# Kernel tuning notes

Hardware: AMD Instinct MI355X
Metric: run time of the kernel (lower is better)

Reference implementation:

```python
import jax, jax.numpy as jnp
import numpy as np

B, D, E, K = 8192, 1024, 8, 5  # batch, in_dim, num_size_classes, num_depth_classes
H = max(64, D)                 # hidden = max(64, in_dim)
EPS = 1e-8


def ordinal_logits_to_probs(logits, num_classes):
    # logits: [B, K-1] cumulative ordinal logits -> [B, K] class probs
    q = jax.nn.sigmoid(logits)
    probs = jnp.concatenate(
        [1.0 - q[:, :1], q[:, :-1] - q[:, 1:], q[:, -1:]], axis=1
    )  # [B, K]
    probs = jnp.clip(probs, EPS)
    return probs / jnp.clip(probs.sum(axis=1, keepdims=True), EPS)


def setup_inputs() -> dict:
    key = jax.random.key(0)
    kx, ks, k1, k2 = jax.random.split(key, 4)
    x = jax.random.normal(kx, (B, D), dtype=jnp.float32)
    size_idx = jax.random.randint(ks, (B,), 0, E, dtype=jnp.int64)
    # per-expert 2-layer MLP params: Linear(D,H) -> ReLU -> Linear(H,K-1)
    W1 = jax.random.normal(k1, (E, D, H), dtype=jnp.float32) / np.sqrt(D)
    b1 = jnp.zeros((E, H), dtype=jnp.float32)
    W2 = jax.random.normal(k2, (E, H, K - 1), dtype=jnp.float32) / np.sqrt(H)
    b2 = jnp.zeros((E, K - 1), dtype=jnp.float32)
    return {"x": x, "size_idx": size_idx, "W1": W1, "b1": b1, "W2": W2, "b2": b2}


def reference(x, size_idx, W1, b1, W2, b2):
    # Hard routing: each token gets the output of expert size_idx[b].
    # Dense all-expert compute + per-token select (same math as mask/gather/scatter,
    # dropout is inference-mode identity).
    h = jax.nn.relu(jnp.einsum('bd,edh->beh', x, W1) + b1)      # [B, E, H]
    all_logits = jnp.einsum('beh,ehk->bek', h, W2) + b2          # [B, E, K-1]
    idx = size_idx.astype(jnp.int32)[:, None, None]              # [B, 1, 1]
    logits = jnp.take_along_axis(all_logits, idx, axis=1)[:, 0]  # [B, K-1]
    probs = ordinal_logits_to_probs(logits, K)                   # [B, K]
    return logits, probs
```

## Files before the change

kernel.cpp:

```cpp
#include <hip/hip_runtime.h>
#include <cstdint>
#include <cstddef>

#define Bn 8192
#define Dn 1024
#define Hn 1024
#define En 8
#define MT 128
#define MTILES (PERM_N / MT)
#define PERM_N (Bn + En * MT)
#define NB 16

#define NXB 4096
#define NWB 2048
#define XB0 1
#define WB0 (XB0 + NXB)
#define TOTB (WB0 + NWB)

typedef unsigned short u16;
typedef __bf16 bf16x8 __attribute__((ext_vector_type(8)));
typedef float f32x4 __attribute__((ext_vector_type(4)));
typedef unsigned short ushort8 __attribute__((ext_vector_type(8)));

__device__ __forceinline__ u16 f2bf(float f) {
  unsigned int u = __float_as_uint(f);
  unsigned int r = u + 0x7fffu + ((u >> 16) & 1u);
  return (u16)(r >> 16);
}

__device__ __forceinline__ void gld16(const void* g, void* l) {
  __builtin_amdgcn_global_load_lds(
      (const __attribute__((address_space(1))) void*)g,
      (__attribute__((address_space(3))) void*)l, 16, 0, 0);
}

#define PIPE_BARRIER_VM4() do {                    \
    asm volatile("" ::: "memory");                 \
    __builtin_amdgcn_s_waitcnt(0x0F74);            \
    __builtin_amdgcn_s_barrier();                  \
    asm volatile("" ::: "memory");                 \
  } while (0)
#define PIPE_BARRIER_VM0() do {                    \
    asm volatile("" ::: "memory");                 \
    __builtin_amdgcn_s_waitcnt(0x0F70);            \
    __builtin_amdgcn_s_barrier();                  \
    asm volatile("" ::: "memory");                 \
  } while (0)

__global__ __launch_bounds__(256) void prep_k(
    const float* __restrict__ x, const int* __restrict__ sidx,
    const float* __restrict__ W1,
    u16* __restrict__ xb, u16* __restrict__ w1t,
    int* __restrict__ off, int* __restrict__ perm) {
  int bid = blockIdx.x;
  int t = threadIdx.x;

  if (bid == 0) {
    __shared__ int hist[4][En];
    __shared__ int base[4][En];
    __shared__ int eoff[En + 1];
    int wv = t >> 6;
    if (t < 4 * En) ((int*)hist)[t] = 0;
#pragma unroll
    for (int i = 0; i < PERM_N / 256; i++) perm[t + i * 256] = -1;
    __syncthreads();
    int e32[32], r32[32];
#pragma unroll
    for (int i = 0; i < 32; i++) {
      int e = sidx[t + i * 256];
      e32[i] = e;
      r32[i] = atomicAdd(&hist[wv][e], 1);
    }
    __syncthreads();
    if (t < En) {
      int s = 0;
      for (int w = 0; w < 4; w++) { base[w][t] = s; s += hist[w][t]; }
      hist[0][t] = s;
    }
    __syncthreads();
    if (t == 0) {
      int o = 0;
      for (int e = 0; e < En; e++) {
        eoff[e] = o; off[e] = o;
        o += (hist[0][e] + MT - 1) & ~(MT - 1);
      }
      eoff[En] = o; off[En] = o;
    }
    __syncthreads();
#pragma unroll
    for (int i = 0; i < 32; i++) {
      int e = e32[i];
      perm[eoff[e] + base[wv][e] + r32[i]] = t + i * 256;
    }
  } else if (bid < WB0) {
    size_t idx = ((size_t)(bid - XB0) * 256 + t) * 8;
    const float* src = x + idx;
    float4 a = *(const float4*)src;
    float4 b = *(const float4*)(src + 4);
    ushort8 o;
    o[0] = f2bf(a.x); o[1] = f2bf(a.y); o[2] = f2bf(a.z); o[3] = f2bf(a.w);
    o[4] = f2bf(b.x); o[5] = f2bf(b.y); o[6] = f2bf(b.z); o[7] = f2bf(b.w);
    *(ushort8*)(xb + idx) = o;
  } else {
    __shared__ float tile[64][65];
    int wb = bid - WB0;
    int e = wb >> 8;
    int k0 = ((wb >> 4) & 15) * 64;
    int n0 = (wb & 15) * 64;
    int c4 = (t & 15) * 4;
    int r0 = t >> 4;
    const float* src = W1 + ((size_t)e << 20) + (size_t)k0 * Hn + n0;
#pragma unroll
    for (int i = 0; i < 4; i++) {
      int r = r0 + i * 16;
      float4 v = *(const float4*)(src + (size_t)r * Hn + c4);
      tile[r][c4 + 0] = v.x; tile[r][c4 + 1] = v.y;
      tile[r][c4 + 2] = v.z; tile[r][c4 + 3] = v.w;
    }
    __syncthreads();
    u16* dst = w1t + ((size_t)e << 20) + (size_t)n0 * Dn + k0;
#pragma unroll
    for (int i = 0; i < 4; i++) {
      int h = r0 + i * 16;
      ushort4 o;
      o.x = f2bf(tile[c4 + 0][h]);
      o.y = f2bf(tile[c4 + 1][h]);
      o.z = f2bf(tile[c4 + 2][h]);
      o.w = f2bf(tile[c4 + 3][h]);
      *(ushort4*)(dst + (size_t)h * Dn + c4) = o;
    }
  }
}

__global__ __launch_bounds__(256) void gemm_k(
    const u16* __restrict__ xb, const u16* __restrict__ w1t,
    const float* __restrict__ b1, const float* __restrict__ w2,
    const int* __restrict__ off, const int* __restrict__ perm,
    float* __restrict__ partials) {
  __shared__ u16 As[3][4096];
  __shared__ u16 Bs[3][4096];

  int n0 = blockIdx.x * 128;
  int row0 = blockIdx.y * MT;
  if (row0 >= off[En]) return;
  int e = 0;
  while (row0 >= off[e + 1]) e++;

  int tid = threadIdx.x;
  int lane = tid & 63, w = tid >> 6;
  int wm = w >> 1, wn = w & 1;

  int srow = lane >> 2;
  int slot = lane & 3;
  int scol = (slot ^ ((srow >> 1) & 3)) * 8;
  const u16* aG[2]; const u16* bG[2];
  int lOff[2];
#pragma unroll
  for (int j = 0; j < 2; j++) {
    int rl = 32 * w + 16 * j + srow;
    int tok = perm[row0 + rl];
    if (tok < 0) tok = 0;
    aG[j] = xb + ((size_t)tok << 10) + scol;
    bG[j] = w1t + ((size_t)e << 20) + (size_t)(n0 + rl) * Dn + scol;
    lOff[j] = (32 * w + 16 * j) * 32;
  }

  f32x4 acc[4][4];
#pragma unroll
  for (int i = 0; i < 4; i++)
#pragma unroll
    for (int j = 0; j < 4; j++)
      acc[i][j] = (f32x4){0.f, 0.f, 0.f, 0.f};

  int fr = lane & 15;
  int qf = lane >> 4;
  int qs = (qf ^ ((fr >> 1) & 3)) * 8;
  int offA[4], offB[4];
#pragma unroll
  for (int i = 0; i < 4; i++)
    offA[i] = (wm * 64 + i * 16 + fr) * 32 + qs;
#pragma unroll
  for (int j = 0; j < 4; j++)
    offB[j] = (wn * 64 + j * 16 + fr) * 32 + qs;

#pragma unroll
  for (int it = 0; it < 2; it++) {
    int ko = it * 32;
    gld16(aG[0] + ko, (u16*)As[it] + lOff[0]);
    gld16(aG[1] + ko, (u16*)As[it] + lOff[1]);
    gld16(bG[0] + ko, (u16*)Bs[it] + lOff[0]);
    gld16(bG[1] + ko, (u16*)Bs[it] + lOff[1]);
  }

#pragma unroll
  for (int i = 0; i < 31; i++) {
    PIPE_BARRIER_VM4();
    if (i + 2 < 32) {
      int s = (i + 2) % 3;
      int ko = (i + 2) * 32;
      gld16(aG[0] + ko, (u16*)As[s] + lOff[0]);
      gld16(aG[1] + ko, (u16*)As[s] + lOff[1]);
      gld16(bG[0] + ko, (u16*)Bs[s] + lOff[0]);
      gld16(bG[1] + ko, (u16*)Bs[s] + lOff[1]);
    }
    const u16* Ab = (const u16*)As[i % 3];
    const u16* Bb = (const u16*)Bs[i % 3];
    bf16x8 af[4], bfr[4];
#pragma unroll
    for (int ii = 0; ii < 4; ii++) af[ii] = *(const bf16x8*)(Ab + offA[ii]);
#pragma unroll
    for (int jj = 0; jj < 4; jj++) bfr[jj] = *(const bf16x8*)(Bb + offB[jj]);
#pragma unroll
    for (int ii = 0; ii < 4; ii++)
#pragma unroll
      for (int jj = 0; jj < 4; jj++)
        acc[ii][jj] = __builtin_amdgcn_mfma_f32_16x16x32_bf16(af[ii], bfr[jj], acc[ii][jj], 0, 0, 0);
  }
  {
    PIPE_BARRIER_VM0();
    const u16* Ab = (const u16*)As[31 % 3];
    const u16* Bb = (const u16*)Bs[31 % 3];
    bf16x8 af[4], bfr[4];
#pragma unroll
    for (int ii = 0; ii < 4; ii++) af[ii] = *(const bf16x8*)(Ab + offA[ii]);
#pragma unroll
    for (int jj = 0; jj < 4; jj++) bfr[jj] = *(const bf16x8*)(Bb + offB[jj]);
#pragma unroll
    for (int ii = 0; ii < 4; ii++)
#pragma unroll
      for (int jj = 0; jj < 4; jj++)
        acc[ii][jj] = __builtin_amdgcn_mfma_f32_16x16x32_bf16(af[ii], bfr[jj], acc[ii][jj], 0, 0, 0);
  }

  int fq = lane >> 4;
  float4 w2v[4]; float b1v[4];
#pragma unroll
  for (int j = 0; j < 4; j++) {
    int col = n0 + wn * 64 + j * 16 + fr;
    w2v[j] = *(const float4*)(w2 + ((size_t)e * Hn + col) * 4);
    b1v[j] = b1[(size_t)e * Hn + col];
  }
  int chunk = blockIdx.x * 2 + wn;
#pragma unroll
  for (int i = 0; i < 4; i++) {
    int rbase = wm * 64 + i * 16 + fq * 4;
#pragma unroll
    for (int r = 0; r < 4; r++) {
      float s0 = 0.f, s1 = 0.f, s2 = 0.f, s3 = 0.f;
#pragma unroll
      for (int j = 0; j < 4; j++) {
        float h = acc[i][j][r] + b1v[j];
        h = fmaxf(h, 0.f);
        s0 = fmaf(h, w2v[j].x, s0);
        s1 = fmaf(h, w2v[j].y, s1);
        s2 = fmaf(h, w2v[j].z, s2);
        s3 = fmaf(h, w2v[j].w, s3);
      }
#pragma unroll
      for (int m = 1; m < 16; m <<= 1) {
        s0 += __shfl_xor(s0, m);
        s1 += __shfl_xor(s1, m);
        s2 += __shfl_xor(s2, m);
        s3 += __shfl_xor(s3, m);
      }
      if (fr == 0) {
        int row = row0 + rbase + r;
        *(float4*)(partials + ((size_t)row * NB + chunk) * 4) =
            make_float4(s0, s1, s2, s3);
      }
    }
  }
}

__global__ void probs_k(const float* __restrict__ partials,
                        const int* __restrict__ perm, const int* __restrict__ off,
                        const int* __restrict__ sidx, const float* __restrict__ b2,
                        float* __restrict__ out) {
  int p = blockIdx.x * blockDim.x + threadIdx.x;
  if (p >= off[En]) return;
  int tok = perm[p];
  if (tok < 0) return;
  int e = sidx[tok];
  float s0 = 0.f, s1 = 0.f, s2 = 0.f, s3 = 0.f;
#pragma unroll
  for (int nb = 0; nb < NB; nb++) {
    float4 v = *(const float4*)(partials + ((size_t)p * NB + nb) * 4);
    s0 += v.x; s1 += v.y; s2 += v.z; s3 += v.w;
  }
  float l0 = s0 + b2[e * 4 + 0];
  float l1 = s1 + b2[e * 4 + 1];
  float l2 = s2 + b2[e * 4 + 2];
  float l3 = s3 + b2[e * 4 + 3];
  out[tok * 4 + 0] = l0; out[tok * 4 + 1] = l1;
  out[tok * 4 + 2] = l2; out[tok * 4 + 3] = l3;
  float q0 = 1.f / (1.f + expf(-l0));
  float q1 = 1.f / (1.f + expf(-l1));
  float q2 = 1.f / (1.f + expf(-l2));
  float q3 = 1.f / (1.f + expf(-l3));
  const float eps = 1e-8f;
  float p0 = fmaxf(1.f - q0, eps);
  float p1 = fmaxf(q0 - q1, eps);
  float p2 = fmaxf(q1 - q2, eps);
  float p3 = fmaxf(q2 - q3, eps);
  float p4 = fmaxf(q3, eps);
  float s = p0 + p1 + p2 + p3 + p4;
  float inv = 1.f / fmaxf(s, eps);
  float* pr = out + (size_t)Bn * 4 + (size_t)tok * 5;
  pr[0] = p0 * inv; pr[1] = p1 * inv; pr[2] = p2 * inv;
  pr[3] = p3 * inv; pr[4] = p4 * inv;
}

extern "C" void kernel_launch(void* const* d_in, const int* in_sizes, int n_in,
                              void* d_out, int out_size, void* d_ws, size_t ws_size,
                              hipStream_t stream) {
  const float* x  = (const float*)d_in[0];
  const int* sidx = (const int*)d_in[1];
  const float* W1 = (const float*)d_in[2];
  const float* b1 = (const float*)d_in[3];
  const float* W2 = (const float*)d_in[4];
  const float* b2 = (const float*)d_in[5];
  float* out = (float*)d_out;

  uint8_t* w = (uint8_t*)d_ws;
  int* off  = (int*)(w + 64);
  int* perm = (int*)(w + 512);
  u16* xb      = (u16*)(w + 40960);
  u16* w1t     = (u16*)(w + 40960 + 16777216);
  float* parts = (float*)(w + 40960 + 2 * 16777216);

  prep_k<<<TOTB, 256, 0, stream>>>(x, sidx, W1, xb, w1t, off, perm);
  gemm_k<<<dim3(Hn / 128, MTILES), 256, 0, stream>>>(xb, w1t, b1, W2, off, perm, parts);
  probs_k<<<(PERM_N + 255) / 256, 256, 0, stream>>>(parts, perm, off, sidx, b2, out);
}
```

Measured before the change: 158.9 us.

## Pre-pack x and W1 into contiguous per-tile KC-chunk layouts for GEMM loads

The x bf16 conversion moves out of prep into a new pack_x kernel that gathers tokens in permuted order and writes them into a tile-blocked layout of 128 rows by 32 K per chunk. The W1 transpose likewise writes a tile-blocked layout, so each GEMM K-step loads one contiguous 8 KB block instead of strided rows and does no perm indirection. This aims to make global-to-LDS loads contiguous and better coalesced. The cost is an extra kernel launch, and pack_x can only start once the permutation is computed, which serialises the x conversion behind the histogram step.

```diff
diff --git a/kernel.cpp b/kernel.cpp
--- a/kernel.cpp
+++ b/kernel.cpp
@@ -7,15 +7,13 @@
 #define Hn 1024
 #define En 8
 #define MT 128
+#define PERM_N (Bn + En * MT)
 #define MTILES (PERM_N / MT)
-#define PERM_N (Bn + En * MT)
 #define NB 16
-
-#define NXB 4096
-#define NWB 2048
-#define XB0 1
-#define WB0 (XB0 + NXB)
-#define TOTB (WB0 + NWB)
+#define KC 32
+#define NKC (Dn / KC)
+#define TSTRIDE (MT * KC)
+#define MT_STRIDE (NKC * TSTRIDE)
 
 typedef unsigned short u16;
 typedef __bf16 bf16x8 __attribute__((ext_vector_type(8)));
@@ -47,11 +45,9 @@
     asm volatile("" ::: "memory");                 \
   } while (0)
 
-__global__ __launch_bounds__(256) void prep_k(
-    const float* __restrict__ x, const int* __restrict__ sidx,
-    const float* __restrict__ W1,
-    u16* __restrict__ xb, u16* __restrict__ w1t,
-    int* __restrict__ off, int* __restrict__ perm) {
+__global__ __launch_bounds__(256) void prep_r(
+    const int* __restrict__ sidx, const float* __restrict__ W1,
+    u16* __restrict__ w1tT, int* __restrict__ off, int* __restrict__ perm) {
   int bid = blockIdx.x;
   int t = threadIdx.x;
 
@@ -92,18 +88,9 @@
       int e = e32[i];
       perm[eoff[e] + base[wv][e] + r32[i]] = t + i * 256;
     }
-  } else if (bid < WB0) {
-    size_t idx = ((size_t)(bid - XB0) * 256 + t) * 8;
-    const float* src = x + idx;
-    float4 a = *(const float4*)src;
-    float4 b = *(const float4*)(src + 4);
-    ushort8 o;
-    o[0] = f2bf(a.x); o[1] = f2bf(a.y); o[2] = f2bf(a.z); o[3] = f2bf(a.w);
-    o[4] = f2bf(b.x); o[5] = f2bf(b.y); o[6] = f2bf(b.z); o[7] = f2bf(b.w);
-    *(ushort8*)(xb + idx) = o;
   } else {
     __shared__ float tile[64][65];
-    int wb = bid - WB0;
+    int wb = bid - 1;
     int e = wb >> 8;
     int k0 = ((wb >> 4) & 15) * 64;
     int n0 = (wb & 15) * 64;
@@ -118,30 +105,63 @@
       tile[r][c4 + 2] = v.z; tile[r][c4 + 3] = v.w;
     }
     __syncthreads();
-    u16* dst = w1t + ((size_t)e << 20) + (size_t)n0 * Dn + k0;
+    u16* dstE = w1tT + ((size_t)e << 20);
 #pragma unroll
     for (int i = 0; i < 4; i++) {
-      int h = r0 + i * 16;
+      int hl = r0 + i * 16;
+      int gh = n0 + hl;
+      int gk = k0 + c4;
+      size_t addr = ((size_t)(gh >> 7) * NKC + (gk >> 5)) * TSTRIDE
+                  + (size_t)(gh & 127) * KC + (gk & 31);
       ushort4 o;
-      o.x = f2bf(tile[c4 + 0][h]);
-      o.y = f2bf(tile[c4 + 1][h]);
-      o.z = f2bf(tile[c4 + 2][h]);
-      o.w = f2bf(tile[c4 + 3][h]);
-      *(ushort4*)(dst + (size_t)h * Dn + c4) = o;
-    }
+      o.x = f2bf(tile[c4 + 0][hl]);
+      o.y = f2bf(tile[c4 + 1][hl]);
+      o.z = f2bf(tile[c4 + 2][hl]);
+      o.w = f2bf(tile[c4 + 3][hl]);
+      *(ushort4*)(dstE + addr) = o;
+    }
+  }
+}
+
+__global__ __launch_bounds__(256) void pack_x(
+    const float* __restrict__ x, const int* __restrict__ perm,
+    const int* __restrict__ off, u16* __restrict__ xbT) {
+  int mt = blockIdx.x, rg = blockIdx.y, t = threadIdx.x;
+  if (mt * MT >= off[En]) return;
+  __shared__ int toks[16];
+  if (t < 16) {
+    int p = perm[mt * MT + rg * 16 + t];
+    toks[t] = p < 0 ? 0 : p;
+  }
+  __syncthreads();
+  u16* dst = xbT + (size_t)mt * MT_STRIDE + (size_t)rg * 16 * KC;
+#pragma unroll
+  for (int i = 0; i < 8; i++) {
+    int v = t + i * 256;
+    int kc = v >> 6;
+    int rem = v & 63;
+    int rl = rem >> 2;
+    int k0 = (rem & 3) * 8;
+    const float* src = x + ((size_t)toks[rl] << 10) + kc * KC + k0;
+    float4 a = *(const float4*)src;
+    float4 b = *(const float4*)(src + 4);
+    ushort8 o;
+    o[0] = f2bf(a.x); o[1] = f2bf(a.y); o[2] = f2bf(a.z); o[3] = f2bf(a.w);
+    o[4] = f2bf(b.x); o[5] = f2bf(b.y); o[6] = f2bf(b.z); o[7] = f2bf(b.w);
+    *(ushort8*)(dst + (size_t)kc * TSTRIDE + rl * KC + k0) = o;
   }
 }
 
 __global__ __launch_bounds__(256) void gemm_k(
-    const u16* __restrict__ xb, const u16* __restrict__ w1t,
+    const u16* __restrict__ xbT, const u16* __restrict__ w1tT,
     const float* __restrict__ b1, const float* __restrict__ w2,
-    const int* __restrict__ off, const int* __restrict__ perm,
-    float* __restrict__ partials) {
+    const int* __restrict__ off, float* __restrict__ partials) {
   __shared__ u16 As[3][4096];
   __shared__ u16 Bs[3][4096];
 
-  int n0 = blockIdx.x * 128;
-  int row0 = blockIdx.y * MT;
+  int nt = blockIdx.x;
+  int mt = blockIdx.y;
+  int row0 = mt * MT;
   if (row0 >= off[En]) return;
   int e = 0;
   while (row0 >= off[e + 1]) e++;
@@ -152,17 +172,15 @@
 
   int srow = lane >> 2;
   int slot = lane & 3;
-  int scol = (slot ^ ((srow >> 1) & 3)) * 8;
-  const u16* aG[2]; const u16* bG[2];
-  int lOff[2];
+  int sx = (slot ^ ((srow >> 1) & 3)) * 8;
+  const u16* aBase = xbT + (size_t)mt * MT_STRIDE;
+  const u16* bBase = w1tT + ((size_t)e << 20) + (size_t)nt * MT_STRIDE;
+  int gOff[2], lOff[2];
 #pragma unroll
   for (int j = 0; j < 2; j++) {
     int rl = 32 * w + 16 * j + srow;
-    int tok = perm[row0 + rl];
-    if (tok < 0) tok = 0;
-    aG[j] = xb + ((size_t)tok << 10) + scol;
-    bG[j] = w1t + ((size_t)e << 20) + (size_t)(n0 + rl) * Dn + scol;
-    lOff[j] = (32 * w + 16 * j) * 32;
+    gOff[j] = rl * KC + sx;
+    lOff[j] = (32 * w + 16 * j) * KC;
   }
 
   f32x4 acc[4][4];
@@ -178,18 +196,18 @@
   int offA[4], offB[4];
 #pragma unroll
   for (int i = 0; i < 4; i++)
-    offA[i] = (wm * 64 + i * 16 + fr) * 32 + qs;
+    offA[i] = (wm * 64 + i * 16 + fr) * KC + qs;
 #pragma unroll
   for (int j = 0; j < 4; j++)
-    offB[j] = (wn * 64 + j * 16 + fr) * 32 + qs;
+    offB[j] = (wn * 64 + j * 16 + fr) * KC + qs;
 
 #pragma unroll
   for (int it = 0; it < 2; it++) {
-    int ko = it * 32;
-    gld16(aG[0] + ko, (u16*)As[it] + lOff[0]);
-    gld16(aG[1] + ko, (u16*)As[it] + lOff[1]);
-    gld16(bG[0] + ko, (u16*)Bs[it] + lOff[0]);
-    gld16(bG[1] + ko, (u16*)Bs[it] + lOff[1]);
+    int ko = it * TSTRIDE;
+    gld16(aBase + ko + gOff[0], (u16*)As[it] + lOff[0]);
+    gld16(aBase + ko + gOff[1], (u16*)As[it] + lOff[1]);
+    gld16(bBase + ko + gOff[0], (u16*)Bs[it] + lOff[0]);
+    gld16(bBase + ko + gOff[1], (u16*)Bs[it] + lOff[1]);
   }
 
 #pragma unroll
@@ -197,11 +215,11 @@
     PIPE_BARRIER_VM4();
     if (i + 2 < 32) {
       int s = (i + 2) % 3;
-      int ko = (i + 2) * 32;
-      gld16(aG[0] + ko, (u16*)As[s] + lOff[0]);
-      gld16(aG[1] + ko, (u16*)As[s] + lOff[1]);
-      gld16(bG[0] + ko, (u16*)Bs[s] + lOff[0]);
-      gld16(bG[1] + ko, (u16*)Bs[s] + lOff[1]);
+      int ko = (i + 2) * TSTRIDE;
+      gld16(aBase + ko + gOff[0], (u16*)As[s] + lOff[0]);
+      gld16(aBase + ko + gOff[1], (u16*)As[s] + lOff[1]);
+      gld16(bBase + ko + gOff[0], (u16*)Bs[s] + lOff[0]);
+      gld16(bBase + ko + gOff[1], (u16*)Bs[s] + lOff[1]);
     }
     const u16* Ab = (const u16*)As[i % 3];
     const u16* Bb = (const u16*)Bs[i % 3];
@@ -233,6 +251,7 @@
   }
 
   int fq = lane >> 4;
+  int n0 = nt * 128;
   float4 w2v[4]; float b1v[4];
 #pragma unroll
   for (int j = 0; j < 4; j++) {
@@ -240,7 +259,7 @@
     w2v[j] = *(const float4*)(w2 + ((size_t)e * Hn + col) * 4);
     b1v[j] = b1[(size_t)e * Hn + col];
   }
-  int chunk = blockIdx.x * 2 + wn;
+  int chunk = nt * 2 + wn;
 #pragma unroll
   for (int i = 0; i < 4; i++) {
     int rbase = wm * 64 + i * 16 + fq * 4;
@@ -324,11 +343,12 @@
   uint8_t* w = (uint8_t*)d_ws;
   int* off  = (int*)(w + 64);
   int* perm = (int*)(w + 512);
-  u16* xb      = (u16*)(w + 40960);
-  u16* w1t     = (u16*)(w + 40960 + 16777216);
-  float* parts = (float*)(w + 40960 + 2 * 16777216);
-
-  prep_k<<<TOTB, 256, 0, stream>>>(x, sidx, W1, xb, w1t, off, perm);
-  gemm_k<<<dim3(Hn / 128, MTILES), 256, 0, stream>>>(xb, w1t, b1, W2, off, perm, parts);
+  u16* xbT     = (u16*)(w + 40960);
+  u16* w1tT    = (u16*)(w + 40960 + 18874368);
+  float* parts = (float*)(w + 40960 + 18874368 + 16777216);
+
+  prep_r<<<2049, 256, 0, stream>>>(sidx, W1, w1tT, off, perm);
+  pack_x<<<dim3(MTILES, 8), 256, 0, stream>>>(x, perm, off, xbT);
+  gemm_k<<<dim3(Hn / 128, MTILES), 256, 0, stream>>>(xbT, w1tT, b1, W2, off, parts);
   probs_k<<<(PERM_N + 255) / 256, 256, 0, stream>>>(parts, perm, off, sidx, b2, out);
 }
```

New measurement: 160.2 us. About the same (+0.8%).

## Deepen GEMM LDS pipeline to four stages and vectorize W1 transpose stores

Applied to the files above, without the earlier changes.

The bf16 GEMM main loop moves from a 3-buffer to a 4-buffer global_load_lds pipeline, keeping two stages in flight (vmcnt 8) to better hide global memory latency. The W1 transpose/convert in the prep kernel now writes 16-byte ushort8 chunks instead of 8-byte ushort4. The extra LDS buffer raises shared memory per block to 64KB, which may cut the number of resident blocks per CU.

```diff
diff --git a/kernel.cpp b/kernel.cpp
--- a/kernel.cpp
+++ b/kernel.cpp
@@ -34,6 +34,12 @@
       (__attribute__((address_space(3))) void*)l, 16, 0, 0);
 }
 
+#define PIPE_BARRIER_VM8() do {                    \
+    asm volatile("" ::: "memory");                 \
+    __builtin_amdgcn_s_waitcnt(0x0F78);            \
+    __builtin_amdgcn_s_barrier();                  \
+    asm volatile("" ::: "memory");                 \
+  } while (0)
 #define PIPE_BARRIER_VM4() do {                    \
     asm volatile("" ::: "memory");                 \
     __builtin_amdgcn_s_waitcnt(0x0F74);            \
@@ -118,16 +124,17 @@
       tile[r][c4 + 2] = v.z; tile[r][c4 + 3] = v.w;
     }
     __syncthreads();
-    u16* dst = w1t + ((size_t)e << 20) + (size_t)n0 * Dn + k0;
-#pragma unroll
-    for (int i = 0; i < 4; i++) {
-      int h = r0 + i * 16;
-      ushort4 o;
-      o.x = f2bf(tile[c4 + 0][h]);
-      o.y = f2bf(tile[c4 + 1][h]);
-      o.z = f2bf(tile[c4 + 2][h]);
-      o.w = f2bf(tile[c4 + 3][h]);
-      *(ushort4*)(dst + (size_t)h * Dn + c4) = o;
+    int kb = t & 7;
+    int h0 = t >> 3;
+    u16* dstE = w1t + ((size_t)e << 20);
+#pragma unroll
+    for (int i = 0; i < 2; i++) {
+      int hl = h0 + i * 32;
+      int gh = n0 + hl;
+      ushort8 o;
+#pragma unroll
+      for (int j = 0; j < 8; j++) o[j] = f2bf(tile[kb * 8 + j][hl]);
+      *(ushort8*)(dstE + (size_t)gh * Dn + k0 + kb * 8) = o;
     }
   }
 }
@@ -137,8 +144,8 @@
     const float* __restrict__ b1, const float* __restrict__ w2,
     const int* __restrict__ off, const int* __restrict__ perm,
     float* __restrict__ partials) {
-  __shared__ u16 As[3][4096];
-  __shared__ u16 Bs[3][4096];
+  __shared__ u16 As[4][4096];
+  __shared__ u16 Bs[4][4096];
 
   int n0 = blockIdx.x * 128;
   int row0 = blockIdx.y * MT;
@@ -183,54 +190,47 @@
   for (int j = 0; j < 4; j++)
     offB[j] = (wn * 64 + j * 16 + fr) * 32 + qs;
 
-#pragma unroll
-  for (int it = 0; it < 2; it++) {
-    int ko = it * 32;
-    gld16(aG[0] + ko, (u16*)As[it] + lOff[0]);
-    gld16(aG[1] + ko, (u16*)As[it] + lOff[1]);
-    gld16(bG[0] + ko, (u16*)Bs[it] + lOff[0]);
-    gld16(bG[1] + ko, (u16*)Bs[it] + lOff[1]);
-  }
-
-#pragma unroll
-  for (int i = 0; i < 31; i++) {
-    PIPE_BARRIER_VM4();
-    if (i + 2 < 32) {
-      int s = (i + 2) % 3;
-      int ko = (i + 2) * 32;
-      gld16(aG[0] + ko, (u16*)As[s] + lOff[0]);
-      gld16(aG[1] + ko, (u16*)As[s] + lOff[1]);
-      gld16(bG[0] + ko, (u16*)Bs[s] + lOff[0]);
-      gld16(bG[1] + ko, (u16*)Bs[s] + lOff[1]);
-    }
-    const u16* Ab = (const u16*)As[i % 3];
-    const u16* Bb = (const u16*)Bs[i % 3];
-    bf16x8 af[4], bfr[4];
-#pragma unroll
-    for (int ii = 0; ii < 4; ii++) af[ii] = *(const bf16x8*)(Ab + offA[ii]);
-#pragma unroll
-    for (int jj = 0; jj < 4; jj++) bfr[jj] = *(const bf16x8*)(Bb + offB[jj]);
-#pragma unroll
-    for (int ii = 0; ii < 4; ii++)
-#pragma unroll
-      for (int jj = 0; jj < 4; jj++)
-        acc[ii][jj] = __builtin_amdgcn_mfma_f32_16x16x32_bf16(af[ii], bfr[jj], acc[ii][jj], 0, 0, 0);
-  }
-  {
-    PIPE_BARRIER_VM0();
-    const u16* Ab = (const u16*)As[31 % 3];
-    const u16* Bb = (const u16*)Bs[31 % 3];
-    bf16x8 af[4], bfr[4];
-#pragma unroll
-    for (int ii = 0; ii < 4; ii++) af[ii] = *(const bf16x8*)(Ab + offA[ii]);
-#pragma unroll
-    for (int jj = 0; jj < 4; jj++) bfr[jj] = *(const bf16x8*)(Bb + offB[jj]);
-#pragma unroll
-    for (int ii = 0; ii < 4; ii++)
-#pragma unroll
-      for (int jj = 0; jj < 4; jj++)
-        acc[ii][jj] = __builtin_amdgcn_mfma_f32_16x16x32_bf16(af[ii], bfr[jj], acc[ii][jj], 0, 0, 0);
-  }
+#define ISSUE_STAGE(st) do {                                          \
+    int _s = (st) & 3;                                                \
+    int _ko = (st) * 32;                                              \
+    gld16(aG[0] + _ko, (u16*)As[_s] + lOff[0]);                       \
+    gld16(aG[1] + _ko, (u16*)As[_s] + lOff[1]);                       \
+    gld16(bG[0] + _ko, (u16*)Bs[_s] + lOff[0]);                       \
+    gld16(bG[1] + _ko, (u16*)Bs[_s] + lOff[1]);                       \
+  } while (0)
+
+#define COMPUTE_STAGE(st) do {                                        \
+    const u16* Ab = (const u16*)As[(st) & 3];                         \
+    const u16* Bb = (const u16*)Bs[(st) & 3];                         \
+    bf16x8 af[4], bfr[4];                                             \
+    _Pragma("unroll")                                                 \
+    for (int ii = 0; ii < 4; ii++) af[ii] = *(const bf16x8*)(Ab + offA[ii]); \
+    _Pragma("unroll")                                                 \
+    for (int jj = 0; jj < 4; jj++) bfr[jj] = *(const bf16x8*)(Bb + offB[jj]); \
+    _Pragma("unroll")                                                 \
+    for (int ii = 0; ii < 4; ii++)                                    \
+      _Pragma("unroll")                                               \
+      for (int jj = 0; jj < 4; jj++)                                  \
+        acc[ii][jj] = __builtin_amdgcn_mfma_f32_16x16x32_bf16(af[ii], bfr[jj], acc[ii][jj], 0, 0, 0); \
+  } while (0)
+
+  ISSUE_STAGE(0);
+  ISSUE_STAGE(1);
+  ISSUE_STAGE(2);
+
+#pragma unroll
+  for (int i = 0; i < 30; i++) {
+    PIPE_BARRIER_VM8();
+    if (i + 3 < 32) ISSUE_STAGE(i + 3);
+    COMPUTE_STAGE(i);
+  }
+  PIPE_BARRIER_VM4();
+  COMPUTE_STAGE(30);
+  PIPE_BARRIER_VM0();
+  COMPUTE_STAGE(31);
+
+#undef ISSUE_STAGE
+#undef COMPUTE_STAGE
 
   int fq = lane >> 4;
   float4 w2v[4]; float b1v[4];
```

Result: slower. 175.4 us (+10.4%).

## Fuse prep, GEMM and probs into one persistent kernel with grid barrier

Applied to the files above, without the earlier changes.

Merges the three kernels into a single launch. Blocks first convert x and W1 to bf16 and build the expert permutation in a grid-stride loop, then meet at a global atomic barrier and run the expert GEMM tiles. The last block to finish each row tile computes the ordinal probabilities, chosen through a per-tile atomic counter. This removes two launch boundaries and the separate probs pass, but it relies on all 576 blocks being co-resident (launch bounds set to 3 blocks per CU) and adds a memset plus spin-waiting.

```diff
diff --git a/kernel.cpp b/kernel.cpp
--- a/kernel.cpp
+++ b/kernel.cpp
@@ -7,15 +7,14 @@
 #define Hn 1024
 #define En 8
 #define MT 128
+#define PERM_N (Bn + En * MT)
 #define MTILES (PERM_N / MT)
-#define PERM_N (Bn + En * MT)
 #define NB 16
+#define NBLK (8 * MTILES)
 
 #define NXB 4096
 #define NWB 2048
-#define XB0 1
-#define WB0 (XB0 + NXB)
-#define TOTB (WB0 + NWB)
+#define NUNITS (NXB + NWB)
 
 typedef unsigned short u16;
 typedef __bf16 bf16x8 __attribute__((ext_vector_type(8)));
@@ -47,18 +46,25 @@
     asm volatile("" ::: "memory");                 \
   } while (0)
 
-__global__ __launch_bounds__(256) void prep_k(
+__global__ __launch_bounds__(256, 3) void fused_k(
     const float* __restrict__ x, const int* __restrict__ sidx,
-    const float* __restrict__ W1,
+    const float* __restrict__ W1, const float* __restrict__ b1,
+    const float* __restrict__ w2, const float* __restrict__ b2,
     u16* __restrict__ xb, u16* __restrict__ w1t,
-    int* __restrict__ off, int* __restrict__ perm) {
-  int bid = blockIdx.x;
+    int* __restrict__ off, int* __restrict__ perm,
+    int* __restrict__ done, int* __restrict__ bar,
+    float* __restrict__ partials, float* __restrict__ out) {
+  __shared__ __align__(16) unsigned char smem[49152];
+
+  int nt = blockIdx.x;
+  int mtb = blockIdx.y;
+  int bid = nt + 8 * mtb;
   int t = threadIdx.x;
 
   if (bid == 0) {
-    __shared__ int hist[4][En];
-    __shared__ int base[4][En];
-    __shared__ int eoff[En + 1];
+    int (*hist)[En] = (int (*)[En])(smem);
+    int (*rbas)[En] = (int (*)[En])(smem + 128);
+    int* eoff = (int*)(smem + 256);
     int wv = t >> 6;
     if (t < 4 * En) ((int*)hist)[t] = 0;
 #pragma unroll
@@ -74,7 +80,7 @@
     __syncthreads();
     if (t < En) {
       int s = 0;
-      for (int w = 0; w < 4; w++) { base[w][t] = s; s += hist[w][t]; }
+      for (int w = 0; w < 4; w++) { rbas[w][t] = s; s += hist[w][t]; }
       hist[0][t] = s;
     }
     __syncthreads();
@@ -90,224 +96,242 @@
 #pragma unroll
     for (int i = 0; i < 32; i++) {
       int e = e32[i];
-      perm[eoff[e] + base[wv][e] + r32[i]] = t + i * 256;
-    }
-  } else if (bid < WB0) {
-    size_t idx = ((size_t)(bid - XB0) * 256 + t) * 8;
-    const float* src = x + idx;
-    float4 a = *(const float4*)src;
-    float4 b = *(const float4*)(src + 4);
-    ushort8 o;
-    o[0] = f2bf(a.x); o[1] = f2bf(a.y); o[2] = f2bf(a.z); o[3] = f2bf(a.w);
-    o[4] = f2bf(b.x); o[5] = f2bf(b.y); o[6] = f2bf(b.z); o[7] = f2bf(b.w);
-    *(ushort8*)(xb + idx) = o;
+      perm[eoff[e] + rbas[wv][e] + r32[i]] = t + i * 256;
+    }
   } else {
-    __shared__ float tile[64][65];
-    int wb = bid - WB0;
-    int e = wb >> 8;
-    int k0 = ((wb >> 4) & 15) * 64;
-    int n0 = (wb & 15) * 64;
-    int c4 = (t & 15) * 4;
-    int r0 = t >> 4;
-    const float* src = W1 + ((size_t)e << 20) + (size_t)k0 * Hn + n0;
+    for (int u = bid - 1; u < NUNITS; u += NBLK - 1) {
+      if (u < NXB) {
+        size_t idx = ((size_t)u * 256 + t) * 8;
+        const float* src = x + idx;
+        float4 a = *(const float4*)src;
+        float4 b = *(const float4*)(src + 4);
+        ushort8 o;
+        o[0] = f2bf(a.x); o[1] = f2bf(a.y); o[2] = f2bf(a.z); o[3] = f2bf(a.w);
+        o[4] = f2bf(b.x); o[5] = f2bf(b.y); o[6] = f2bf(b.z); o[7] = f2bf(b.w);
+        *(ushort8*)(xb + idx) = o;
+      } else {
+        __syncthreads();
+        float (*tile)[65] = (float (*)[65])(smem);
+        int wb = u - NXB;
+        int e = wb >> 8;
+        int k0 = ((wb >> 4) & 15) * 64;
+        int n0 = (wb & 15) * 64;
+        int c4 = (t & 15) * 4;
+        int r0 = t >> 4;
+        const float* src = W1 + ((size_t)e << 20) + (size_t)k0 * Hn + n0;
+#pragma unroll
+        for (int i = 0; i < 4; i++) {
+          int r = r0 + i * 16;
+          float4 v = *(const float4*)(src + (size_t)r * Hn + c4);
+          tile[r][c4 + 0] = v.x; tile[r][c4 + 1] = v.y;
+          tile[r][c4 + 2] = v.z; tile[r][c4 + 3] = v.w;
+        }
+        __syncthreads();
+        u16* dst = w1t + ((size_t)e << 20) + (size_t)n0 * Dn + k0;
+#pragma unroll
+        for (int i = 0; i < 4; i++) {
+          int h = r0 + i * 16;
+          ushort4 o;
+          o.x = f2bf(tile[c4 + 0][h]);
+          o.y = f2bf(tile[c4 + 1][h]);
+          o.z = f2bf(tile[c4 + 2][h]);
+          o.w = f2bf(tile[c4 + 3][h]);
+          *(ushort4*)(dst + (size_t)h * Dn + c4) = o;
+        }
+      }
+    }
+  }
+
+  __syncthreads();
+  if (t == 0) {
+    __threadfence();
+    __hip_atomic_fetch_add(&bar[0], 1, __ATOMIC_RELAXED, __HIP_MEMORY_SCOPE_AGENT);
+    while (__hip_atomic_load(&bar[0], __ATOMIC_RELAXED, __HIP_MEMORY_SCOPE_AGENT) < NBLK)
+      __builtin_amdgcn_s_sleep(8);
+    __threadfence();
+  }
+  __syncthreads();
+
+  int n0g = nt * 128;
+  int row0 = mtb * MT;
+  bool live = (row0 < off[En]);
+  if (live) {
+    u16 (*As)[4096] = (u16 (*)[4096])(smem);
+    u16 (*Bs)[4096] = (u16 (*)[4096])(smem + 24576);
+    int e = 0;
+    while (row0 >= off[e + 1]) e++;
+
+    int lane = t & 63, w = t >> 6;
+    int wm = w >> 1, wn = w & 1;
+
+    int srow = lane >> 2;
+    int slot = lane & 3;
+    int scol = (slot ^ ((srow >> 1) & 3)) * 8;
+    const u16* aG[2]; const u16* bG[2];
+    int lOff[2];
+#pragma unroll
+    for (int j = 0; j < 2; j++) {
+      int rl = 32 * w + 16 * j + srow;
+      int tok = perm[row0 + rl];
+      if (tok < 0) tok = 0;
+      aG[j] = xb + ((size_t)tok << 10) + scol;
+      bG[j] = w1t + ((size_t)e << 20) + (size_t)(n0g + rl) * Dn + scol;
+      lOff[j] = (32 * w + 16 * j) * 32;
+    }
+
+    f32x4 acc[4][4];
+#pragma unroll
+    for (int i = 0; i < 4; i++)
+#pragma unroll
+      for (int j = 0; j < 4; j++)
+        acc[i][j] = (f32x4){0.f, 0.f, 0.f, 0.f};
+
+    int fr = lane & 15;
+    int qf = lane >> 4;
+    int qs = (qf ^ ((fr >> 1) & 3)) * 8;
+    int offA[4], offB[4];
+#pragma unroll
+    for (int i = 0; i < 4; i++)
+      offA[i] = (wm * 64 + i * 16 + fr) * 32 + qs;
+#pragma unroll
+    for (int j = 0; j < 4; j++)
+      offB[j] = (wn * 64 + j * 16 + fr) * 32 + qs;
+
+#pragma unroll
+    for (int it = 0; it < 2; it++) {
+      int ko = it * 32;
+      gld16(aG[0] + ko, (u16*)As[it] + lOff[0]);
+      gld16(aG[1] + ko, (u16*)As[it] + lOff[1]);
+      gld16(bG[0] + ko, (u16*)Bs[it] + lOff[0]);
+      gld16(bG[1] + ko, (u16*)Bs[it] + lOff[1]);
+    }
+
+#pragma unroll
+    for (int i = 0; i < 31; i++) {
+      PIPE_BARRIER_VM4();
+      if (i + 2 < 32) {
+        int s = (i + 2) % 3;
+        int ko = (i + 2) * 32;
+        gld16(aG[0] + ko, (u16*)As[s] + lOff[0]);
+        gld16(aG[1] + ko, (u16*)As[s] + lOff[1]);
+        gld16(bG[0] + ko, (u16*)Bs[s] + lOff[0]);
+        gld16(bG[1] + ko, (u16*)Bs[s] + lOff[1]);
+      }
+      const u16* Ab = (const u16*)As[i % 3];
+      const u16* Bb = (const u16*)Bs[i % 3];
+      bf16x8 af[4], bfr[4];
+#pragma unroll
+      for (int ii = 0; ii < 4; ii++) af[ii] = *(const bf16x8*)(Ab + offA[ii]);
+#pragma unroll
+      for (int jj = 0; jj < 4; jj++) bfr[jj] = *(const bf16x8*)(Bb + offB[jj]);
+#pragma unroll
+      for (int ii = 0; ii < 4; ii++)
+#pragma unroll
+        for (int jj = 0; jj < 4; jj++)
+          acc[ii][jj] = __builtin_amdgcn_mfma_f32_16x16x32_bf16(af[ii], bfr[jj], acc[ii][jj], 0, 0, 0);
+    }
+    {
+      PIPE_BARRIER_VM0();
+      const u16* Ab = (const u16*)As[31 % 3];
+      const u16* Bb = (const u16*)Bs[31 % 3];
+      bf16x8 af[4], bfr[4];
+#pragma unroll
+      for (int ii = 0; ii < 4; ii++) af[ii] = *(const bf16x8*)(Ab + offA[ii]);
+#pragma unroll
+      for (int jj = 0; jj < 4; jj++) bfr[jj] = *(const bf16x8*)(Bb + offB[jj]);
+#pragma unroll
+      for (int ii = 0; ii < 4; ii++)
+#pragma unroll
+        for (int jj = 0; jj < 4; jj++)
+          acc[ii][jj] = __builtin_amdgcn_mfma_f32_16x16x32_bf16(af[ii], bfr[jj], acc[ii][jj], 0, 0, 0);
+    }
+
+    int fq = lane >> 4;
+    float4 w2v[4]; float b1v[4];
+#pragma unroll
+    for (int j = 0; j < 4; j++) {
+      int col = n0g + wn * 64 + j * 16 + fr;
+      w2v[j] = *(const float4*)(w2 + ((size_t)e * Hn + col) * 4);
+      b1v[j] = b1[(size_t)e * Hn + col];
+    }
+    int chunk = nt * 2 + wn;
 #pragma unroll
     for (int i = 0; i < 4; i++) {
-      int r = r0 + i * 16;
-      float4 v = *(const float4*)(src + (size_t)r * Hn + c4);
-      tile[r][c4 + 0] = v.x; tile[r][c4 + 1] = v.y;
-      tile[r][c4 + 2] = v.z; tile[r][c4 + 3] = v.w;
-    }
-    __syncthreads();
-    u16* dst = w1t + ((size_t)e << 20) + (size_t)n0 * Dn + k0;
-#pragma unroll
-    for (int i = 0; i < 4; i++) {
-      int h = r0 + i * 16;
-      ushort4 o;
-      o.x = f2bf(tile[c4 + 0][h]);
-      o.y = f2bf(tile[c4 + 1][h]);
-      o.z = f2bf(tile[c4 + 2][h]);
-      o.w = f2bf(tile[c4 + 3][h]);
-      *(ushort4*)(dst + (size_t)h * Dn + c4) = o;
+      int rbase = wm * 64 + i * 16 + fq * 4;
+#pragma unroll
+      for (int r = 0; r < 4; r++) {
+        float s0 = 0.f, s1 = 0.f, s2 = 0.f, s3 = 0.f;
+#pragma unroll
+        for (int j = 0; j < 4; j++) {
+          float h = acc[i][j][r] + b1v[j];
+          h = fmaxf(h, 0.f);
+          s0 = fmaf(h, w2v[j].x, s0);
+          s1 = fmaf(h, w2v[j].y, s1);
+          s2 = fmaf(h, w2v[j].z, s2);
+          s3 = fmaf(h, w2v[j].w, s3);
+        }
+#pragma unroll
+        for (int m = 1; m < 16; m <<= 1) {
+          s0 += __shfl_xor(s0, m);
+          s1 += __shfl_xor(s1, m);
+          s2 += __shfl_xor(s2, m);
+          s3 += __shfl_xor(s3, m);
+        }
+        if (fr == 0) {
+          int row = row0 + rbase + r;
+          *(float4*)(partials + ((size_t)row * NB + chunk) * 4) =
+              make_float4(s0, s1, s2, s3);
+        }
+      }
+    }
+
+    __threadfence();
+    __syncthreads();
+    int* win = (int*)smem;
+    if (t == 0) {
+      int k = __hip_atomic_fetch_add(&done[mtb], 1, __ATOMIC_SEQ_CST,
+                                     __HIP_MEMORY_SCOPE_AGENT);
+      *win = (k == 7) ? 1 : 0;
+    }
+    __syncthreads();
+    if (*win) {
+      __threadfence();
+      if (t < MT) {
+        int p = row0 + t;
+        int tok = perm[p];
+        if (tok >= 0) {
+          int ex = sidx[tok];
+          float s0 = 0.f, s1 = 0.f, s2 = 0.f, s3 = 0.f;
+#pragma unroll
+          for (int nb = 0; nb < NB; nb++) {
+            float4 v = *(const float4*)(partials + ((size_t)p * NB + nb) * 4);
+            s0 += v.x; s1 += v.y; s2 += v.z; s3 += v.w;
+          }
+          float l0 = s0 + b2[ex * 4 + 0];
+          float l1 = s1 + b2[ex * 4 + 1];
+          float l2 = s2 + b2[ex * 4 + 2];
+          float l3 = s3 + b2[ex * 4 + 3];
+          out[tok * 4 + 0] = l0; out[tok * 4 + 1] = l1;
+          out[tok * 4 + 2] = l2; out[tok * 4 + 3] = l3;
+          float q0 = 1.f / (1.f + expf(-l0));
+          float q1 = 1.f / (1.f + expf(-l1));
+          float q2 = 1.f / (1.f + expf(-l2));
+          float q3 = 1.f / (1.f + expf(-l3));
+          const float eps = 1e-8f;
+          float p0 = fmaxf(1.f - q0, eps);
+          float p1 = fmaxf(q0 - q1, eps);
+          float p2 = fmaxf(q1 - q2, eps);
+          float p3 = fmaxf(q2 - q3, eps);
+          float p4 = fmaxf(q3, eps);
+          float s = p0 + p1 + p2 + p3 + p4;
+          float inv = 1.f / fmaxf(s, eps);
+          float* pr = out + (size_t)Bn * 4 + (size_t)tok * 5;
+          pr[0] = p0 * inv; pr[1] = p1 * inv; pr[2] = p2 * inv;
+          pr[3] = p3 * inv; pr[4] = p4 * inv;
+        }
+      }
     }
   }
-}
-
-__global__ __launch_bounds__(256) void gemm_k(
-    const u16* __restrict__ xb, const u16* __restrict__ w1t,
-    const float* __restrict__ b1, const float* __restrict__ w2,
-    const int* __restrict__ off, const int* __restrict__ perm,
-    float* __restrict__ partials) {
-  __shared__ u16 As[3][4096];
-  __shared__ u16 Bs[3][4096];
-
-  int n0 = blockIdx.x * 128;
-  int row0 = blockIdx.y * MT;
-  if (row0 >= off[En]) return;
-  int e = 0;
-  while (row0 >= off[e + 1]) e++;
-
-  int tid = threadIdx.x;
-  int lane = tid & 63, w = tid >> 6;
-  int wm = w >> 1, wn = w & 1;
-
-  int srow = lane >> 2;
-  int slot = lane & 3;
-  int scol = (slot ^ ((srow >> 1) & 3)) * 8;
-  const u16* aG[2]; const u16* bG[2];
-  int lOff[2];
-#pragma unroll
-  for (int j = 0; j < 2; j++) {
-    int rl = 32 * w + 16 * j + srow;
-    int tok = perm[row0 + rl];
-    if (tok < 0) tok = 0;
-    aG[j] = xb + ((size_t)tok << 10) + scol;
-    bG[j] = w1t + ((size_t)e << 20) + (size_t)(n0 + rl) * Dn + scol;
-    lOff[j] = (32 * w + 16 * j) * 32;
-  }
-
-  f32x4 acc[4][4];
-#pragma unroll
-  for (int i = 0; i < 4; i++)
-#pragma unroll
-    for (int j = 0; j < 4; j++)
-      acc[i][j] = (f32x4){0.f, 0.f, 0.f, 0.f};
-
-  int fr = lane & 15;
-  int qf = lane >> 4;
-  int qs = (qf ^ ((fr >> 1) & 3)) * 8;
-  int offA[4], offB[4];
-#pragma unroll
-  for (int i = 0; i < 4; i++)
-    offA[i] = (wm * 64 + i * 16 + fr) * 32 + qs;
-#pragma unroll
-  for (int j = 0; j < 4; j++)
-    offB[j] = (wn * 64 + j * 16 + fr) * 32 + qs;
-
-#pragma unroll
-  for (int it = 0; it < 2; it++) {
-    int ko = it * 32;
-    gld16(aG[0] + ko, (u16*)As[it] + lOff[0]);
-    gld16(aG[1] + ko, (u16*)As[it] + lOff[1]);
-    gld16(bG[0] + ko, (u16*)Bs[it] + lOff[0]);
-    gld16(bG[1] + ko, (u16*)Bs[it] + lOff[1]);
-  }
-
-#pragma unroll
-  for (int i = 0; i < 31; i++) {
-    PIPE_BARRIER_VM4();
-    if (i + 2 < 32) {
-      int s = (i + 2) % 3;
-      int ko = (i + 2) * 32;
-      gld16(aG[0] + ko, (u16*)As[s] + lOff[0]);
-      gld16(aG[1] + ko, (u16*)As[s] + lOff[1]);
-      gld16(bG[0] + ko, (u16*)Bs[s] + lOff[0]);
-      gld16(bG[1] + ko, (u16*)Bs[s] + lOff[1]);
-    }
-    const u16* Ab = (const u16*)As[i % 3];
-    const u16* Bb = (const u16*)Bs[i % 3];
-    bf16x8 af[4], bfr[4];
-#pragma unroll
-    for (int ii = 0; ii < 4; ii++) af[ii] = *(const bf16x8*)(Ab + offA[ii]);
-#pragma unroll
-    for (int jj = 0; jj < 4; jj++) bfr[jj] = *(const bf16x8*)(Bb + offB[jj]);
-#pragma unroll
-    for (int ii = 0; ii < 4; ii++)
-#pragma unroll
-      for (int jj = 0; jj < 4; jj++)
-        acc[ii][jj] = __builtin_amdgcn_mfma_f32_16x16x32_bf16(af[ii], bfr[jj], acc[ii][jj], 0, 0, 0);
-  }
-  {
-    PIPE_BARRIER_VM0();
-    const u16* Ab = (const u16*)As[31 % 3];
-    const u16* Bb = (const u16*)Bs[31 % 3];
-    bf16x8 af[4], bfr[4];
-#pragma unroll
-    for (int ii = 0; ii < 4; ii++) af[ii] = *(const bf16x8*)(Ab + offA[ii]);
-#pragma unroll
-    for (int jj = 0; jj < 4; jj++) bfr[jj] = *(const bf16x8*)(Bb + offB[jj]);
-#pragma unroll
-    for (int ii = 0; ii < 4; ii++)
-#pragma unroll
-      for (int jj = 0; jj < 4; jj++)
-        acc[ii][jj] = __builtin_amdgcn_mfma_f32_16x16x32_bf16(af[ii], bfr[jj], acc[ii][jj], 0, 0, 0);
-  }
-
-  int fq = lane >> 4;
-  float4 w2v[4]; float b1v[4];
-#pragma unroll
-  for (int j = 0; j < 4; j++) {
-    int col = n0 + wn * 64 + j * 16 + fr;
-    w2v[j] = *(const float4*)(w2 + ((size_t)e * Hn + col) * 4);
-    b1v[j] = b1[(size_t)e * Hn + col];
-  }
-  int chunk = blockIdx.x * 2 + wn;
-#pragma unroll
-  for (int i = 0; i < 4; i++) {
-    int rbase = wm * 64 + i * 16 + fq * 4;
-#pragma unroll
-    for (int r = 0; r < 4; r++) {
-      float s0 = 0.f, s1 = 0.f, s2 = 0.f, s3 = 0.f;
-#pragma unroll
-      for (int j = 0; j < 4; j++) {
-        float h = acc[i][j][r] + b1v[j];
-        h = fmaxf(h, 0.f);
-        s0 = fmaf(h, w2v[j].x, s0);
-        s1 = fmaf(h, w2v[j].y, s1);
-        s2 = fmaf(h, w2v[j].z, s2);
-        s3 = fmaf(h, w2v[j].w, s3);
-      }
-#pragma unroll
-      for (int m = 1; m < 16; m <<= 1) {
-        s0 += __shfl_xor(s0, m);
-        s1 += __shfl_xor(s1, m);
-        s2 += __shfl_xor(s2, m);
-        s3 += __shfl_xor(s3, m);
-      }
-      if (fr == 0) {
-        int row = row0 + rbase + r;
-        *(float4*)(partials + ((size_t)row * NB + chunk) * 4) =
-            make_float4(s0, s1, s2, s3);
-      }
-    }
-  }
-}
-
-__global__ void probs_k(const float* __restrict__ partials,
-                        const int* __restrict__ perm, const int* __restrict__ off,
-                        const int* __restrict__ sidx, const float* __restrict__ b2,
-                        float* __restrict__ out) {
-  int p = blockIdx.x * blockDim.x + threadIdx.x;
-  if (p >= off[En]) return;
-  int tok = perm[p];
-  if (tok < 0) return;
-  int e = sidx[tok];
-  float s0 = 0.f, s1 = 0.f, s2 = 0.f, s3 = 0.f;
-#pragma unroll
-  for (int nb = 0; nb < NB; nb++) {
-    float4 v = *(const float4*)(partials + ((size_t)p * NB + nb) * 4);
-    s0 += v.x; s1 += v.y; s2 += v.z; s3 += v.w;
-  }
-  float l0 = s0 + b2[e * 4 + 0];
-  float l1 = s1 + b2[e * 4 + 1];
-  float l2 = s2 + b2[e * 4 + 2];
-  float l3 = s3 + b2[e * 4 + 3];
-  out[tok * 4 + 0] = l0; out[tok * 4 + 1] = l1;
-  out[tok * 4 + 2] = l2; out[tok * 4 + 3] = l3;
-  float q0 = 1.f / (1.f + expf(-l0));
-  float q1 = 1.f / (1.f + expf(-l1));
-  float q2 = 1.f / (1.f + expf(-l2));
-  float q3 = 1.f / (1.f + expf(-l3));
-  const float eps = 1e-8f;
-  float p0 = fmaxf(1.f - q0, eps);
-  float p1 = fmaxf(q0 - q1, eps);
-  float p2 = fmaxf(q1 - q2, eps);
-  float p3 = fmaxf(q2 - q3, eps);
-  float p4 = fmaxf(q3, eps);
-  float s = p0 + p1 + p2 + p3 + p4;
-  float inv = 1.f / fmaxf(s, eps);
-  float* pr = out + (size_t)Bn * 4 + (size_t)tok * 5;
-  pr[0] = p0 * inv; pr[1] = p1 * inv; pr[2] = p2 * inv;
-  pr[3] = p3 * inv; pr[4] = p4 * inv;
 }
 
 extern "C" void kernel_launch(void* const* d_in, const int* in_sizes, int n_in,
@@ -322,13 +346,15 @@
   float* out = (float*)d_out;
 
   uint8_t* w = (uint8_t*)d_ws;
-  int* off  = (int*)(w + 64);
+  int* done = (int*)(w + 0);
+  int* bar  = (int*)(w + 288);
+  int* off  = (int*)(w + 320);
   int* perm = (int*)(w + 512);
   u16* xb      = (u16*)(w + 40960);
   u16* w1t     = (u16*)(w + 40960 + 16777216);
   float* parts = (float*)(w + 40960 + 2 * 16777216);
 
-  prep_k<<<TOTB, 256, 0, stream>>>(x, sidx, W1, xb, w1t, off, perm);
-  gemm_k<<<dim3(Hn / 128, MTILES), 256, 0, stream>>>(xb, w1t, b1, W2, off, perm, parts);
-  probs_k<<<(PERM_N + 255) / 256, 256, 0, stream>>>(parts, perm, off, sidx, b2, out);
+  hipMemsetAsync(w, 0, 512, stream);
+  fused_k<<<dim3(8, MTILES), 256, 0, stream>>>(
+      x, sidx, W1, b1, W2, b2, xb, w1t, off, perm, done, bar, parts, out);
 }
```

After: 304.6 us. +91.7%, slower.
